# Performance work log

Measured on AMD Instinct MI355X. Metric: run time of the kernel, lower is better.

The kernel has to match this reference:

```python
import jax, jax.numpy as jnp
import numpy as np

B, S, H = 1, 2048, 4608
NH, NKV, HD = 36, 4, 128
GROUP = NH // NKV  # 9
ROPE_THETA = 100000.0
SLIDING_WINDOW = 1024


def _rope_tables(seq_len, head_dim):
    inv_freq = 1.0 / (ROPE_THETA ** (jnp.arange(0, head_dim, 2, dtype=jnp.float32) / head_dim))
    ang = jnp.arange(seq_len, dtype=jnp.float32)[:, None] * inv_freq[None, :]  # [S, HD/2]
    emb = jnp.concatenate([ang, ang], axis=-1)  # [S, HD]
    return jnp.cos(emb), jnp.sin(emb)


def setup_inputs() -> dict:
    key = jax.random.key(0)
    ks = jax.random.split(key, 10)
    std = 0.02
    cos_table, sin_table = _rope_tables(S, HD)
    return {
        "hidden_states": jax.random.normal(ks[0], (B, S, H), jnp.float32),
        "position_ids": jnp.broadcast_to(jnp.arange(S, dtype=jnp.int64)[None, :], (B, S)),
        "cos_table": cos_table,
        "sin_table": sin_table,
        "q_w": jax.random.normal(ks[1], (NH * HD, H), jnp.float32) * std,
        "q_b": jax.random.normal(ks[2], (NH * HD,), jnp.float32) * std,
        "k_w": jax.random.normal(ks[3], (NKV * HD, H), jnp.float32) * std,
        "k_b": jax.random.normal(ks[4], (NKV * HD,), jnp.float32) * std,
        "v_w": jax.random.normal(ks[5], (NKV * HD, H), jnp.float32) * std,
        "v_b": jax.random.normal(ks[6], (NKV * HD,), jnp.float32) * std,
        "o_w": jax.random.normal(ks[7], (H, NH * HD), jnp.float32) * std,
        "o_b": jax.random.normal(ks[8], (H,), jnp.float32) * std,
        "sliding_window": SLIDING_WINDOW,
    }


def _rotate_half(x):
    x1, x2 = jnp.split(x, 2, axis=-1)
    return jnp.concatenate([-x2, x1], axis=-1)


def reference(hidden_states, position_ids, cos_table, sin_table,
              q_w, q_b, k_w, k_b, v_w, v_b, o_w, o_b, sliding_window):
    bsz, q_len, _ = hidden_states.shape
    scaling = HD ** -0.5

    q = (hidden_states @ q_w.T + q_b).reshape(bsz, q_len, NH, HD)
    k = (hidden_states @ k_w.T + k_b).reshape(bsz, q_len, NKV, HD)
    v = (hidden_states @ v_w.T + v_b).reshape(bsz, q_len, NKV, HD)

    # RoPE with explicit cos/sin, unsqueeze_dim=2 ('bsnd' layout)
    cos = cos_table[position_ids][:, :, None, :]  # [B, S, 1, HD]
    sin = sin_table[position_ids][:, :, None, :]
    q = q * cos + _rotate_half(q) * sin
    k = k * cos + _rotate_half(k) * sin

    # GQA: group Q heads per KV head
    qg = q.reshape(bsz, q_len, NKV, GROUP, HD)
    logits = jnp.einsum('bqgrd,bkgd->bgrqk', qg, k) * scaling  # [B, NKV, GROUP, S, S]

    # causal + sliding-window mask: attend where k <= q and q - k < window
    idx = jnp.arange(q_len)
    mask = (idx[:, None] >= idx[None, :]) & (idx[:, None] - idx[None, :] < sliding_window)
    logits = jnp.where(mask[None, None, None, :, :], logits, jnp.finfo(logits.dtype).min)

    probs = jax.nn.softmax(logits, axis=-1)
    attn = jnp.einsum('bgrqk,bkgd->bqgrd', probs, v).reshape(bsz, q_len, NH * HD)
    return attn @ o_w.T + o_b
```

## Files before the change

### kernel.cpp

```cpp
#include <hip/hip_runtime.h>
#include <stdint.h>

typedef __attribute__((ext_vector_type(8))) __bf16 bf16x8;
typedef __attribute__((ext_vector_type(4))) float f32x4;
typedef __attribute__((ext_vector_type(8))) unsigned short u16x8;
typedef __attribute__((ext_vector_type(4))) unsigned short u16x4;

#define SEQ 2048
#define HID 4608
#define NQKV 5632
#define NHEAD 36
#define NKVH 4
#define HDIM 128
#define WINDOW 1024

__device__ __forceinline__ unsigned short f2b(float f) {
    unsigned u = __builtin_bit_cast(unsigned, f);
    u += 0x7fffu + ((u >> 16) & 1u);
    return (unsigned short)(u >> 16);
}
__device__ __forceinline__ float b2f(unsigned short h) {
    unsigned u = ((unsigned)h) << 16;
    return __builtin_bit_cast(float, u);
}

#define GLD16(gp, lp) __builtin_amdgcn_global_load_lds( \
    (const __attribute__((address_space(1))) void*)(gp), \
    (__attribute__((address_space(3))) void*)(lp), 16, 0, 0)

#define VMCNT8() asm volatile("s_waitcnt vmcnt(8)" ::: "memory")
#define VMCNT7() asm volatile("s_waitcnt vmcnt(7)" ::: "memory")
#define VMCNT5() asm volatile("s_waitcnt vmcnt(5)" ::: "memory")
#define VMCNT4() asm volatile("s_waitcnt vmcnt(4)" ::: "memory")
#define VMCNT0() asm volatile("s_waitcnt vmcnt(0)" ::: "memory")
#define BARRIER() asm volatile("s_barrier" ::: "memory")

__global__ __launch_bounds__(256) void conv_all_kernel(
    const float* __restrict__ s0, unsigned short* __restrict__ d0, int n0,
    const float* __restrict__ s1, unsigned short* __restrict__ d1, int n1,
    const float* __restrict__ s2, unsigned short* __restrict__ d2, int n2,
    const float* __restrict__ s3, unsigned short* __restrict__ d3, int n3)
{
    int total = n0 + n1 + n2 + n3;
    int stride = gridDim.x * blockDim.x;
    for (int i = blockIdx.x * blockDim.x + threadIdx.x; i < total; i += stride) {
        const float* src; unsigned short* dst; int j = i;
        if (j < n0) { src = s0; dst = d0; }
        else if ((j -= n0) < n1) { src = s1; dst = d1; }
        else if ((j -= n1) < n2) { src = s2; dst = d2; }
        else { j -= n2; src = s3; dst = d3; }
        float4 v = ((const float4*)src)[j];
        ushort4 o;
        o.x = f2b(v.x); o.y = f2b(v.y); o.z = f2b(v.z); o.w = f2b(v.w);
        ((ushort4*)dst)[j] = o;
    }
}

__global__ __launch_bounds__(512, 2) void gemm256_kernel(
    const unsigned short* __restrict__ A,
    const unsigned short* __restrict__ W,
    void* __restrict__ out,
    const float* __restrict__ b0, const float* __restrict__ b1, const float* __restrict__ b2,
    int N, int K, int GX, int GB, int outf32,
    const float* __restrict__ cw_src, unsigned short* __restrict__ cw_dst, int cw_n4)
{
    const int tid = threadIdx.x;
    const int o = blockIdx.x;

    if (o >= GB) {
        int cb = o - GB, ncb = gridDim.x - GB;
        int stride = ncb * 512;
        for (int i = cb * 512 + tid; i < cw_n4; i += stride) {
            float4 v = ((const float4*)cw_src)[i];
            ushort4 u;
            u.x = f2b(v.x); u.y = f2b(v.y); u.z = f2b(v.z); u.w = f2b(v.w);
            ((ushort4*)cw_dst)[i] = u;
        }
        return;
    }

    __shared__ alignas(16) unsigned short ldsA[2][256 * 64];
    __shared__ alignas(16) unsigned short ldsB[2][256 * 64];

    const int w = tid >> 6, lane = tid & 63;
    const int r16 = lane & 15, kg = lane >> 4;
    const int wm = w >> 2, wn = w & 3;

    const int cpx = GB >> 3;
    const int id = (o & 7) * cpx + (o >> 3);
    const int bx = id % GX, by = id / GX;
    const int row0 = by * 256, col0 = bx * 256;

    const int lr = lane >> 3;
    const int lc = lane & 7;
    const int cg = lc ^ lr;
    const unsigned short* Abase = A + (size_t)row0 * K;
    const unsigned short* Wbase = W + (size_t)col0 * K;

    auto STG = [&](const unsigned short* Mat, unsigned short* ldsSlot, int hf, int kb) {
#pragma unroll
        for (int j = 0; j < 2; ++j) {
            int row = hf * 128 + (w * 2 + j) * 8 + lr;
            GLD16(Mat + (size_t)row * K + kb + cg * 8,
                  (char*)ldsSlot + hf * 16384 + (w * 2 + j) * 1024);
        }
    };

    const int NITER = K >> 7;
    f32x4 acc[8][4] = {};
    const int swz = r16 & 7;

    bf16x8 af[4][2], bfA[2][2], bfB[2][2];

#define DSR_A(mh, Sl) \
_Pragma("unroll") for (int mi = 0; mi < 4; ++mi) \
_Pragma("unroll") for (int kh = 0; kh < 2; ++kh) \
    af[mi][kh] = *(const bf16x8*)((Sl) + (wm * 128 + (mh) * 64 + mi * 16 + r16) * 64 + ((kh * 4 + kg) ^ swz) * 8);
#define DSR_B(nh, Sl, BF) \
_Pragma("unroll") for (int ni = 0; ni < 2; ++ni) \
_Pragma("unroll") for (int kh = 0; kh < 2; ++kh) \
    BF[ni][kh] = *(const bf16x8*)((Sl) + (wn * 64 + (nh) * 32 + ni * 16 + r16) * 64 + ((kh * 4 + kg) ^ swz) * 8);
#define MFMA_Q(mh, nh, BF) \
    asm volatile("s_waitcnt lgkmcnt(0)" ::: "memory"); \
    __builtin_amdgcn_sched_barrier(0); \
    __builtin_amdgcn_s_setprio(1); \
_Pragma("unroll") for (int mi = 0; mi < 4; ++mi) \
_Pragma("unroll") for (int ni = 0; ni < 2; ++ni) \
_Pragma("unroll") for (int kh = 0; kh < 2; ++kh) \
    acc[(mh) * 4 + mi][(nh) * 2 + ni] = __builtin_amdgcn_mfma_f32_16x16x32_bf16(af[mi][kh], BF[ni][kh], acc[(mh) * 4 + mi][(nh) * 2 + ni], 0, 0, 0); \
    __builtin_amdgcn_s_setprio(0); \
    __builtin_amdgcn_sched_barrier(0);

    STG(Abase, ldsA[0], 0, 0);  STG(Abase, ldsA[0], 1, 0);
    STG(Wbase, ldsB[0], 0, 0);  STG(Wbase, ldsB[0], 1, 0);
    STG(Abase, ldsA[1], 0, 64); STG(Abase, ldsA[1], 1, 64);
    STG(Wbase, ldsB[1], 0, 64); STG(Wbase, ldsB[1], 1, 64);
    VMCNT0();
    BARRIER();

    for (int i = 0; i < NITER; ++i) {
        const unsigned short* A0 = ldsA[0];
        const unsigned short* B0 = ldsB[0];
        const unsigned short* A1 = ldsA[1];
        const unsigned short* B1 = ldsB[1];
        const bool st = (i + 1 < NITER);
        const int kb0 = (i + 1) * 128;
        const int kb1 = kb0 + 64;

        DSR_A(0, A0); DSR_B(0, B0, bfA);
        BARRIER();
        MFMA_Q(0, 0, bfA);
        BARRIER();
        DSR_B(1, B0, bfB);
        BARRIER();
        MFMA_Q(0, 1, bfB);
        BARRIER();
        DSR_A(1, A0);
        if (st) STG(Wbase, ldsB[0], 0, kb0);
        BARRIER();
        MFMA_Q(1, 1, bfB);
        BARRIER();
        if (st) { STG(Abase, ldsA[0], 0, kb0); VMCNT4(); } else { VMCNT0(); }
        BARRIER();
        MFMA_Q(1, 0, bfA);
        BARRIER();
        DSR_A(0, A1); DSR_B(0, B1, bfA);
        if (st) STG(Abase, ldsA[0], 1, kb0);
        BARRIER();
        MFMA_Q(0, 0, bfA);
        BARRIER();
        DSR_B(1, B1, bfB);
        if (st) STG(Wbase, ldsB[0], 1, kb0);
        BARRIER();
        MFMA_Q(0, 1, bfB);
        BARRIER();
        DSR_A(1, A1);
        if (st) { STG(Wbase, ldsB[1], 0, kb1); STG(Wbase, ldsB[1], 1, kb1); }
        BARRIER();
        MFMA_Q(1, 1, bfB);
        BARRIER();
        if (st) { STG(Abase, ldsA[1], 0, kb1); STG(Abase, ldsA[1], 1, kb1); VMCNT8(); }
        BARRIER();
        MFMA_Q(1, 0, bfA);
        BARRIER();
    }

    if (!outf32) {
        unsigned short* O = (unsigned short*)out;
#pragma unroll
        for (int m = 0; m < 8; ++m)
#pragma unroll
            for (int n = 0; n < 4; ++n)
#pragma unroll
                for (int r = 0; r < 4; ++r) {
                    int row = row0 + wm * 128 + m * 16 + kg * 4 + r;
                    int col = col0 + wn * 64 + n * 16 + r16;
                    float bias = (col < HID) ? b0[col]
                               : (col < HID + 512 ? b1[col - HID] : b2[col - HID - 512]);
                    O[(size_t)row * N + col] = f2b(acc[m][n][r] + bias);
                }
    } else {
        float* O = (float*)out;
#pragma unroll
        for (int m = 0; m < 8; ++m)
#pragma unroll
            for (int n = 0; n < 4; ++n)
#pragma unroll
                for (int r = 0; r < 4; ++r) {
                    int row = row0 + wm * 128 + m * 16 + kg * 4 + r;
                    int col = col0 + wn * 64 + n * 16 + r16;
                    O[(size_t)row * N + col] = acc[m][n][r] + b0[col];
                }
    }
#undef DSR_A
#undef DSR_B
#undef MFMA_Q
}

__global__ __launch_bounds__(512, 1) void gemm192_kernel(
    const unsigned short* __restrict__ A,
    const unsigned short* __restrict__ W,
    float* __restrict__ out,
    const float* __restrict__ b0,
    int N, int K, int GX)
{
    __shared__ alignas(16) unsigned short ldsA[2][256 * 64];
    __shared__ alignas(16) unsigned short ldsB[2][192 * 64];

    const int tid = threadIdx.x;
    const int w = tid >> 6, lane = tid & 63;
    const int r16 = lane & 15, kg = lane >> 4;
    const int wm = w >> 2, wn = w & 3;

    const int cpx = gridDim.x >> 3;
    const int o = blockIdx.x;
    const int id = (o & 7) * cpx + (o >> 3);
    const int bx = id % GX, by = id / GX;
    const int row0 = by * 256, col0 = bx * 192;

    const int lr = lane >> 3;
    const int lc = lane & 7;
    const int cg = lc ^ lr;
    const unsigned short* Abase = A + (size_t)row0 * K;
    const unsigned short* Wbase = W + (size_t)col0 * K;

    auto STGA = [&](unsigned short* slot, int hf, int kb) {
#pragma unroll
        for (int j = 0; j < 2; ++j) {
            int row = hf * 128 + (w * 2 + j) * 8 + lr;
            GLD16(Abase + (size_t)row * K + kb + cg * 8,
                  (char*)slot + hf * 16384 + (w * 2 + j) * 1024);
        }
    };
    auto STGB = [&](unsigned short* slot, int j3, int kb) {
        int row = j3 * 64 + w * 8 + lr;
        GLD16(Wbase + (size_t)row * K + kb + cg * 8,
              (char*)slot + j3 * 8192 + w * 1024);
    };

    const int NITER = K >> 7;
    f32x4 acc[8][3] = {};
    const int swz = r16 & 7;

    bf16x8 af[4][2], bf2[2][2], bf1[2];

#define DSR_A(mh, Sl) \
_Pragma("unroll") for (int mi = 0; mi < 4; ++mi) \
_Pragma("unroll") for (int kh = 0; kh < 2; ++kh) \
    af[mi][kh] = *(const bf16x8*)((Sl) + (wm * 128 + (mh) * 64 + mi * 16 + r16) * 64 + ((kh * 4 + kg) ^ swz) * 8);
#define DSR_B2(Sl) \
_Pragma("unroll") for (int ni = 0; ni < 2; ++ni) \
_Pragma("unroll") for (int kh = 0; kh < 2; ++kh) \
    bf2[ni][kh] = *(const bf16x8*)((Sl) + (wn * 48 + ni * 16 + r16) * 64 + ((kh * 4 + kg) ^ swz) * 8);
#define DSR_B1(Sl) \
_Pragma("unroll") for (int kh = 0; kh < 2; ++kh) \
    bf1[kh] = *(const bf16x8*)((Sl) + (wn * 48 + 32 + r16) * 64 + ((kh * 4 + kg) ^ swz) * 8);
#define MFMA_Q2(mh) \
    asm volatile("s_waitcnt lgkmcnt(0)" ::: "memory"); \
    __builtin_amdgcn_sched_barrier(0); \
    __builtin_amdgcn_s_setprio(1); \
_Pragma("unroll") for (int mi = 0; mi < 4; ++mi) \
_Pragma("unroll") for (int ni = 0; ni < 2; ++ni) \
_Pragma("unroll") for (int kh = 0; kh < 2; ++kh) \
    acc[(mh) * 4 + mi][ni] = __builtin_amdgcn_mfma_f32_16x16x32_bf16(af[mi][kh], bf2[ni][kh], acc[(mh) * 4 + mi][ni], 0, 0, 0); \
    __builtin_amdgcn_s_setprio(0); \
    __builtin_amdgcn_sched_barrier(0);
#define MFMA_Q1(mh) \
    asm volatile("s_waitcnt lgkmcnt(0)" ::: "memory"); \
    __builtin_amdgcn_sched_barrier(0); \
    __builtin_amdgcn_s_setprio(1); \
_Pragma("unroll") for (int mi = 0; mi < 4; ++mi) \
_Pragma("unroll") for (int kh = 0; kh < 2; ++kh) \
    acc[(mh) * 4 + mi][2] = __builtin_amdgcn_mfma_f32_16x16x32_bf16(af[mi][kh], bf1[kh], acc[(mh) * 4 + mi][2], 0, 0, 0); \
    __builtin_amdgcn_s_setprio(0); \
    __builtin_amdgcn_sched_barrier(0);

    STGA(ldsA[0], 0, 0);  STGA(ldsA[0], 1, 0);
    STGB(ldsB[0], 0, 0);  STGB(ldsB[0], 1, 0);  STGB(ldsB[0], 2, 0);
    STGA(ldsA[1], 0, 64); STGA(ldsA[1], 1, 64);
    STGB(ldsB[1], 0, 64); STGB(ldsB[1], 1, 64); STGB(ldsB[1], 2, 64);
    VMCNT0();
    BARRIER();

    for (int i = 0; i < NITER; ++i) {
        const unsigned short* A0 = ldsA[0];
        const unsigned short* B0 = ldsB[0];
        const unsigned short* A1 = ldsA[1];
        const unsigned short* B1 = ldsB[1];
        const bool st = (i + 1 < NITER);
        const int kb0 = (i + 1) * 128;
        const int kb1 = kb0 + 64;

        DSR_A(0, A0); DSR_B2(B0);
        BARRIER();
        MFMA_Q2(0);
        BARRIER();
        DSR_B1(B0);
        BARRIER();
        MFMA_Q1(0);
        BARRIER();
        DSR_A(1, A0);
        if (st) { STGB(ldsB[0], 0, kb0); STGB(ldsB[0], 1, kb0); STGB(ldsB[0], 2, kb0); }
        BARRIER();
        MFMA_Q1(1);
        BARRIER();
        if (st) { STGA(ldsA[0], 0, kb0); VMCNT5(); } else { VMCNT0(); }
        BARRIER();
        MFMA_Q2(1);
        BARRIER();
        DSR_A(0, A1); DSR_B2(B1);
        if (st) STGA(ldsA[0], 1, kb0);
        BARRIER();
        MFMA_Q2(0);
        BARRIER();
        DSR_B1(B1);
        BARRIER();
        MFMA_Q1(0);
        BARRIER();
        DSR_A(1, A1);
        if (st) { STGB(ldsB[1], 0, kb1); STGB(ldsB[1], 1, kb1); STGB(ldsB[1], 2, kb1);
                  STGA(ldsA[1], 0, kb1); }
        BARRIER();
        MFMA_Q1(1);
        BARRIER();
        if (st) { STGA(ldsA[1], 1, kb1); VMCNT7(); }
        BARRIER();
        MFMA_Q2(1);
        BARRIER();
    }

#pragma unroll
    for (int m = 0; m < 8; ++m)
#pragma unroll
        for (int n = 0; n < 3; ++n)
#pragma unroll
            for (int r = 0; r < 4; ++r) {
                int row = row0 + wm * 128 + m * 16 + kg * 4 + r;
                int col = col0 + wn * 48 + n * 16 + r16;
                out[(size_t)row * N + col] = acc[m][n][r] + b0[col];
            }
#undef DSR_A
#undef DSR_B2
#undef DSR_B1
#undef MFMA_Q2
#undef MFMA_Q1
}

__global__ __launch_bounds__(256) void rope_kernel(unsigned short* __restrict__ qkv,
                                                   const float* __restrict__ cos_t,
                                                   const float* __restrict__ sin_t) {
    int idx = blockIdx.x * 256 + threadIdx.x;
    int d = idx & 63;
    int t = idx >> 6;
    int head = t % 40;
    int s = t / 40;
    int base = head < NHEAD ? head * HDIM : HID + (head - NHEAD) * HDIM;
    size_t off = (size_t)s * NQKV + base;
    float x = b2f(qkv[off + d]);
    float y = b2f(qkv[off + d + 64]);
    float c = cos_t[s * HDIM + d];
    float sn = sin_t[s * HDIM + d];
    qkv[off + d]      = f2b(x * c - y * sn);
    qkv[off + d + 64] = f2b(y * c + x * sn);
}

__global__ __launch_bounds__(256) void vtrans_kernel(const unsigned short* __restrict__ qkv,
                                                     unsigned short* __restrict__ vtg) {
    __shared__ unsigned short tile[32][36];
    const int s0 = blockIdx.x * 32, d0 = blockIdx.y * 32, kvh = blockIdx.z;
    const int lid = threadIdx.x;
    {
        int sl = lid >> 3, dc = (lid & 7) * 4;
        u16x4 v = *(const u16x4*)(qkv + (size_t)(s0 + sl) * NQKV + HID + 512 + kvh * HDIM + d0 + dc);
#pragma unroll
        for (int i = 0; i < 4; ++i) tile[sl][dc + i] = v[i];
    }
    __syncthreads();
    {
        int dl = lid >> 3, sc = (lid & 7) * 4;
        u16x4 v;
#pragma unroll
        for (int i = 0; i < 4; ++i) v[i] = tile[sc + i][dl];
        *(u16x4*)(vtg + (size_t)kvh * HDIM * SEQ + (size_t)(d0 + dl) * SEQ + s0 + sc) = v;
    }
}

#define KSTR 136
#define VSTR 72
#define PSTR 88
__global__ __launch_bounds__(256) void attn_kernel(const unsigned short* __restrict__ qkv,
                                                   const unsigned short* __restrict__ vtg,
                                                   unsigned short* __restrict__ aout)
{
    __shared__ alignas(16) unsigned short Ks[64 * KSTR];
    __shared__ alignas(16) unsigned short Vt[128 * VSTR];
    __shared__ alignas(16) unsigned short Ps[4 * 16 * PSTR];
    const int h = blockIdx.x, qb = blockIdx.y;
    const int q0 = qb * 64;
    const int kvh = h / 9;
    const int tid = threadIdx.x, wid = tid >> 6, lane = tid & 63;
    const int r16 = lane & 15, kg = lane >> 4;
    const int qbase = q0 + wid * 16;
    const unsigned short* vsrc = vtg + (size_t)kvh * HDIM * SEQ;

    bf16x8 qf[4];
    {
        const unsigned short* qrow = qkv + (size_t)(qbase + r16) * NQKV + h * HDIM;
#pragma unroll
        for (int kk = 0; kk < 4; ++kk)
            qf[kk] = *(const bf16x8*)(qrow + kk * 32 + kg * 8);
    }

    f32x4 o[8] = {};
    float mrow[4], lrow[4];
#pragma unroll
    for (int r = 0; r < 4; ++r) { mrow[r] = -1e30f; lrow[r] = 0.f; }

    int lo = q0 - (WINDOW - 1); if (lo < 0) lo = 0; lo &= ~63;
    unsigned short* myP = Ps + wid * 16 * PSTR;
    const float scale = 0.08838834764831845f;

    u16x8 kreg[4], vreg[4];
#define PREF(KT) \
_Pragma("unroll") for (int j = 0; j < 4; ++j) { \
        int c = tid + j * 256; \
        int key = c >> 4, dc = c & 15; \
        kreg[j] = *(const u16x8*)(qkv + (size_t)((KT) + key) * NQKV + HID + kvh * HDIM + dc * 8); \
        int d = c >> 3, k8 = (c & 7) * 8; \
        vreg[j] = *(const u16x8*)(vsrc + (size_t)d * SEQ + (KT) + k8); \
    }

    PREF(lo);

    for (int kt = lo; kt <= q0; kt += 64) {
#pragma unroll
        for (int j = 0; j < 4; ++j) {
            int c = tid + j * 256;
            int key = c >> 4, dc = c & 15;
            *(u16x8*)(Ks + key * KSTR + dc * 8) = kreg[j];
            int d = c >> 3, k8 = (c & 7) * 8;
            *(u16x8*)(Vt + d * VSTR + k8) = vreg[j];
        }
        __syncthreads();

        if (kt + 64 <= q0) { PREF(kt + 64); }

        f32x4 sc[4] = {};
#pragma unroll
        for (int t = 0; t < 4; ++t)
#pragma unroll
            for (int kk = 0; kk < 4; ++kk) {
                bf16x8 kf = *(const bf16x8*)(Ks + (t * 16 + r16) * KSTR + kk * 32 + kg * 8);
                sc[t] = __builtin_amdgcn_mfma_f32_16x16x32_bf16(qf[kk], kf, sc[t], 0, 0, 0);
            }

        float p[4][4], mt[4];
#pragma unroll
        for (int r = 0; r < 4; ++r) mt[r] = -1e30f;
#pragma unroll
        for (int t = 0; t < 4; ++t)
#pragma unroll
            for (int r = 0; r < 4; ++r) {
                int q = qbase + kg * 4 + r;
                int key = kt + t * 16 + r16;
                bool valid = (key <= q) && (q - key < WINDOW);
                float v = valid ? sc[t][r] * scale : -1e30f;
                p[t][r] = v;
                mt[r] = fmaxf(mt[r], v);
            }
#pragma unroll
        for (int mask = 1; mask <= 8; mask <<= 1)
#pragma unroll
            for (int r = 0; r < 4; ++r)
                mt[r] = fmaxf(mt[r], __shfl_xor(mt[r], mask, 64));

        float alpha[4], tsum[4];
#pragma unroll
        for (int r = 0; r < 4; ++r) {
            float mnew = fmaxf(mrow[r], mt[r]);
            alpha[r] = __expf(mrow[r] - mnew);
            mrow[r] = mnew;
            tsum[r] = 0.f;
        }
#pragma unroll
        for (int t = 0; t < 4; ++t)
#pragma unroll
            for (int r = 0; r < 4; ++r) {
                float e = __expf(p[t][r] - mrow[r]);
                p[t][r] = e;
                tsum[r] += e;
            }
#pragma unroll
        for (int mask = 1; mask <= 8; mask <<= 1)
#pragma unroll
            for (int r = 0; r < 4; ++r)
                tsum[r] += __shfl_xor(tsum[r], mask, 64);
#pragma unroll
        for (int r = 0; r < 4; ++r)
            lrow[r] = lrow[r] * alpha[r] + tsum[r];
#pragma unroll
        for (int n = 0; n < 8; ++n)
#pragma unroll
            for (int r = 0; r < 4; ++r)
                o[n][r] = o[n][r] * alpha[r];

#pragma unroll
        for (int t = 0; t < 4; ++t)
#pragma unroll
            for (int r = 0; r < 4; ++r)
                myP[(kg * 4 + r) * PSTR + t * 16 + r16] = f2b(p[t][r]);
        asm volatile("s_waitcnt lgkmcnt(0)" ::: "memory");

#pragma unroll
        for (int kc = 0; kc < 2; ++kc) {
            bf16x8 pa = *(const bf16x8*)(myP + r16 * PSTR + kc * 32 + kg * 8);
#pragma unroll
            for (int n = 0; n < 8; ++n) {
                bf16x8 vb = *(const bf16x8*)(Vt + (n * 16 + r16) * VSTR + kc * 32 + kg * 8);
                o[n] = __builtin_amdgcn_mfma_f32_16x16x32_bf16(pa, vb, o[n], 0, 0, 0);
            }
        }
        BARRIER();
    }
#undef PREF

#pragma unroll
    for (int n = 0; n < 8; ++n)
#pragma unroll
        for (int r = 0; r < 4; ++r) {
            int q = qbase + kg * 4 + r;
            aout[(size_t)q * HID + h * HDIM + n * 16 + r16] = f2b(o[n][r] / lrow[r]);
        }
}

extern "C" void kernel_launch(void* const* d_in, const int* in_sizes, int n_in,
                              void* d_out, int out_size, void* d_ws, size_t ws_size,
                              hipStream_t stream) {
    const float* hidden = (const float*)d_in[0];
    const float* cos_t = (const float*)d_in[2];
    const float* sin_t = (const float*)d_in[3];
    const float* q_w = (const float*)d_in[4];
    const float* q_b = (const float*)d_in[5];
    const float* k_w = (const float*)d_in[6];
    const float* k_b = (const float*)d_in[7];
    const float* v_w = (const float*)d_in[8];
    const float* v_b = (const float*)d_in[9];
    const float* o_w = (const float*)d_in[10];
    const float* o_b = (const float*)d_in[11];

    char* ws = (char*)d_ws;
    unsigned short* hbf  = (unsigned short*)ws;
    unsigned short* attn = hbf;
    unsigned short* wqkv = (unsigned short*)(ws + 18874368);
    unsigned short* vtg  = wqkv;
    unsigned short* wo   = (unsigned short*)(ws + 70778880);
    unsigned short* qkv  = (unsigned short*)(ws + 113246208);

    dim3 blk(256);
    conv_all_kernel<<<4096, blk, 0, stream>>>(
        hidden, hbf,                          (SEQ * HID) / 4,
        q_w,    wqkv,                         (HID * HID) / 4,
        k_w,    wqkv + (size_t)HID * HID,     (512 * HID) / 4,
        v_w,    wqkv + (size_t)5120 * HID,    (512 * HID) / 4);

    gemm256_kernel<<<dim3(256), dim3(512), 0, stream>>>(
        hbf, wqkv, qkv, q_b, k_b, v_b, NQKV, HID, 22, 176, 0,
        o_w, wo, (HID * HID) / 4);
    rope_kernel<<<(SEQ * 40 * 64) / 256, blk, 0, stream>>>(qkv, cos_t, sin_t);
    vtrans_kernel<<<dim3(SEQ / 32, HDIM / 32, NKVH), blk, 0, stream>>>(qkv, vtg);
    attn_kernel<<<dim3(NHEAD, SEQ / 64), blk, 0, stream>>>(qkv, vtg, attn);
    gemm192_kernel<<<dim3(192), dim3(512), 0, stream>>>(
        attn, wo, (float*)d_out, o_b, HID, HID, 24);
}
```

Measured before the change: 407.5 us.

## Fuse RoPE with V transpose and double attention query tile to 128 rows

RoPE and the V transpose now run as one launch: blocks below 5120 apply vectorized RoPE on four elements each, and the remaining blocks transpose V. The attention kernel moves to 512 threads with 128 query rows per block, so each K/V tile loaded to shared memory serves twice as many queries. The key loop extends to q0+64 to cover the extra rows. A mask-free path is added for tiles that are fully inside the causal window. The cost is fewer, larger blocks, which may lower occupancy and waste some work on diagonal tiles.

New measurement: 413.4 us. About the same (+1.5%).

```diff
diff --git a/kernel.cpp b/kernel.cpp
--- a/kernel.cpp
+++ b/kernel.cpp
@@ -366,57 +366,67 @@
 #undef MFMA_Q1
 }
 
-__global__ __launch_bounds__(256) void rope_kernel(unsigned short* __restrict__ qkv,
-                                                   const float* __restrict__ cos_t,
-                                                   const float* __restrict__ sin_t) {
-    int idx = blockIdx.x * 256 + threadIdx.x;
-    int d = idx & 63;
-    int t = idx >> 6;
-    int head = t % 40;
-    int s = t / 40;
-    int base = head < NHEAD ? head * HDIM : HID + (head - NHEAD) * HDIM;
-    size_t off = (size_t)s * NQKV + base;
-    float x = b2f(qkv[off + d]);
-    float y = b2f(qkv[off + d + 64]);
-    float c = cos_t[s * HDIM + d];
-    float sn = sin_t[s * HDIM + d];
-    qkv[off + d]      = f2b(x * c - y * sn);
-    qkv[off + d + 64] = f2b(y * c + x * sn);
-}
-
-__global__ __launch_bounds__(256) void vtrans_kernel(const unsigned short* __restrict__ qkv,
-                                                     unsigned short* __restrict__ vtg) {
-    __shared__ unsigned short tile[32][36];
-    const int s0 = blockIdx.x * 32, d0 = blockIdx.y * 32, kvh = blockIdx.z;
-    const int lid = threadIdx.x;
-    {
-        int sl = lid >> 3, dc = (lid & 7) * 4;
-        u16x4 v = *(const u16x4*)(qkv + (size_t)(s0 + sl) * NQKV + HID + 512 + kvh * HDIM + d0 + dc);
-#pragma unroll
-        for (int i = 0; i < 4; ++i) tile[sl][dc + i] = v[i];
-    }
-    __syncthreads();
-    {
-        int dl = lid >> 3, sc = (lid & 7) * 4;
-        u16x4 v;
-#pragma unroll
-        for (int i = 0; i < 4; ++i) v[i] = tile[sc + i][dl];
-        *(u16x4*)(vtg + (size_t)kvh * HDIM * SEQ + (size_t)(d0 + dl) * SEQ + s0 + sc) = v;
+__global__ __launch_bounds__(256) void rope_vt_kernel(unsigned short* __restrict__ qkv,
+                                                      const float* __restrict__ cos_t,
+                                                      const float* __restrict__ sin_t,
+                                                      unsigned short* __restrict__ vtg) {
+    const int bid = blockIdx.x;
+    if (bid < 5120) {
+        int idx = bid * 256 + threadIdx.x;
+        int d4 = idx & 15;
+        int t2 = idx >> 4;
+        int head = t2 % 40;
+        int s = t2 / 40;
+        int base = head < NHEAD ? head * HDIM : HID + (head - NHEAD) * HDIM;
+        size_t off = (size_t)s * NQKV + base + d4 * 4;
+        u16x4 xv = *(const u16x4*)(qkv + off);
+        u16x4 yv = *(const u16x4*)(qkv + off + 64);
+        float4 c = *(const float4*)(cos_t + s * HDIM + d4 * 4);
+        float4 sn = *(const float4*)(sin_t + s * HDIM + d4 * 4);
+        u16x4 xo, yo;
+        float x, y;
+        x = b2f(xv[0]); y = b2f(yv[0]); xo[0] = f2b(x * c.x - y * sn.x); yo[0] = f2b(y * c.x + x * sn.x);
+        x = b2f(xv[1]); y = b2f(yv[1]); xo[1] = f2b(x * c.y - y * sn.y); yo[1] = f2b(y * c.y + x * sn.y);
+        x = b2f(xv[2]); y = b2f(yv[2]); xo[2] = f2b(x * c.z - y * sn.z); yo[2] = f2b(y * c.z + x * sn.z);
+        x = b2f(xv[3]); y = b2f(yv[3]); xo[3] = f2b(x * c.w - y * sn.w); yo[3] = f2b(y * c.w + x * sn.w);
+        *(u16x4*)(qkv + off) = xo;
+        *(u16x4*)(qkv + off + 64) = yo;
+    } else {
+        __shared__ unsigned short tile[32][36];
+        int vb = bid - 5120;
+        const int s0 = (vb & 63) * 32;
+        const int d0 = ((vb >> 6) & 3) * 32;
+        const int kvh = vb >> 8;
+        const int lid = threadIdx.x;
+        {
+            int sl = lid >> 3, dc = (lid & 7) * 4;
+            u16x4 v = *(const u16x4*)(qkv + (size_t)(s0 + sl) * NQKV + HID + 512 + kvh * HDIM + d0 + dc);
+#pragma unroll
+            for (int i = 0; i < 4; ++i) tile[sl][dc + i] = v[i];
+        }
+        __syncthreads();
+        {
+            int dl = lid >> 3, sc = (lid & 7) * 4;
+            u16x4 v;
+#pragma unroll
+            for (int i = 0; i < 4; ++i) v[i] = tile[sc + i][dl];
+            *(u16x4*)(vtg + (size_t)kvh * HDIM * SEQ + (size_t)(d0 + dl) * SEQ + s0 + sc) = v;
+        }
     }
 }
 
 #define KSTR 136
 #define VSTR 72
 #define PSTR 88
-__global__ __launch_bounds__(256) void attn_kernel(const unsigned short* __restrict__ qkv,
+__global__ __launch_bounds__(512) void attn_kernel(const unsigned short* __restrict__ qkv,
                                                    const unsigned short* __restrict__ vtg,
                                                    unsigned short* __restrict__ aout)
 {
     __shared__ alignas(16) unsigned short Ks[64 * KSTR];
     __shared__ alignas(16) unsigned short Vt[128 * VSTR];
-    __shared__ alignas(16) unsigned short Ps[4 * 16 * PSTR];
+    __shared__ alignas(16) unsigned short Ps[8 * 16 * PSTR];
     const int h = blockIdx.x, qb = blockIdx.y;
-    const int q0 = qb * 64;
+    const int q0 = qb * 128;
     const int kvh = h / 9;
     const int tid = threadIdx.x, wid = tid >> 6, lane = tid & 63;
     const int r16 = lane & 15, kg = lane >> 4;
@@ -437,13 +447,14 @@
     for (int r = 0; r < 4; ++r) { mrow[r] = -1e30f; lrow[r] = 0.f; }
 
     int lo = q0 - (WINDOW - 1); if (lo < 0) lo = 0; lo &= ~63;
+    const int hi = q0 + 64;
     unsigned short* myP = Ps + wid * 16 * PSTR;
     const float scale = 0.08838834764831845f;
 
-    u16x8 kreg[4], vreg[4];
+    u16x8 kreg[2], vreg[2];
 #define PREF(KT) \
-_Pragma("unroll") for (int j = 0; j < 4; ++j) { \
-        int c = tid + j * 256; \
+_Pragma("unroll") for (int j = 0; j < 2; ++j) { \
+        int c = tid + j * 512; \
         int key = c >> 4, dc = c & 15; \
         kreg[j] = *(const u16x8*)(qkv + (size_t)((KT) + key) * NQKV + HID + kvh * HDIM + dc * 8); \
         int d = c >> 3, k8 = (c & 7) * 8; \
@@ -452,10 +463,10 @@
 
     PREF(lo);
 
-    for (int kt = lo; kt <= q0; kt += 64) {
-#pragma unroll
-        for (int j = 0; j < 4; ++j) {
-            int c = tid + j * 256;
+    for (int kt = lo; kt <= hi; kt += 64) {
+#pragma unroll
+        for (int j = 0; j < 2; ++j) {
+            int c = tid + j * 512;
             int key = c >> 4, dc = c & 15;
             *(u16x8*)(Ks + key * KSTR + dc * 8) = kreg[j];
             int d = c >> 3, k8 = (c & 7) * 8;
@@ -463,7 +474,7 @@
         }
         __syncthreads();
 
-        if (kt + 64 <= q0) { PREF(kt + 64); }
+        if (kt + 64 <= hi) { PREF(kt + 64); }
 
         f32x4 sc[4] = {};
 #pragma unroll
@@ -477,17 +488,29 @@
         float p[4][4], mt[4];
 #pragma unroll
         for (int r = 0; r < 4; ++r) mt[r] = -1e30f;
-#pragma unroll
-        for (int t = 0; t < 4; ++t)
-#pragma unroll
-            for (int r = 0; r < 4; ++r) {
-                int q = qbase + kg * 4 + r;
-                int key = kt + t * 16 + r16;
-                bool valid = (key <= q) && (q - key < WINDOW);
-                float v = valid ? sc[t][r] * scale : -1e30f;
-                p[t][r] = v;
-                mt[r] = fmaxf(mt[r], v);
-            }
+        const bool fullv = (kt + 63 <= qbase) && (qbase + 15 - kt < WINDOW);
+        if (fullv) {
+#pragma unroll
+            for (int t = 0; t < 4; ++t)
+#pragma unroll
+                for (int r = 0; r < 4; ++r) {
+                    float v = sc[t][r] * scale;
+                    p[t][r] = v;
+                    mt[r] = fmaxf(mt[r], v);
+                }
+        } else {
+#pragma unroll
+            for (int t = 0; t < 4; ++t)
+#pragma unroll
+                for (int r = 0; r < 4; ++r) {
+                    int q = qbase + kg * 4 + r;
+                    int key = kt + t * 16 + r16;
+                    bool valid = (key <= q) && (q - key < WINDOW);
+                    float v = valid ? sc[t][r] * scale : -1e30f;
+                    p[t][r] = v;
+                    mt[r] = fmaxf(mt[r], v);
+                }
+        }
 #pragma unroll
         for (int mask = 1; mask <= 8; mask <<= 1)
 #pragma unroll
@@ -586,9 +609,8 @@
     gemm256_kernel<<<dim3(256), dim3(512), 0, stream>>>(
         hbf, wqkv, qkv, q_b, k_b, v_b, NQKV, HID, 22, 176, 0,
         o_w, wo, (HID * HID) / 4);
-    rope_kernel<<<(SEQ * 40 * 64) / 256, blk, 0, stream>>>(qkv, cos_t, sin_t);
-    vtrans_kernel<<<dim3(SEQ / 32, HDIM / 32, NKVH), blk, 0, stream>>>(qkv, vtg);
-    attn_kernel<<<dim3(NHEAD, SEQ / 64), blk, 0, stream>>>(qkv, vtg, attn);
+    rope_vt_kernel<<<6144, blk, 0, stream>>>(qkv, cos_t, sin_t, vtg);
+    attn_kernel<<<dim3(NHEAD, SEQ / 128), dim3(512), 0, stream>>>(qkv, vtg, attn);
     gemm192_kernel<<<dim3(192), dim3(512), 0, stream>>>(
         attn, wo, (float*)d_out, o_b, HID, HID, 24);
 }
```
